# Performance work log

Hardware: AMD Instinct MI355X
Metric: run time of the kernel (lower is better)

The kernel has to match this reference:

```python
import jax, jax.numpy as jnp
import numpy as np

B, T, D = 4, 2048, 1024
H = 16
HD = D // H


def setup_inputs() -> dict:
    key = jax.random.key(0)
    ks = jax.random.split(key, 6)
    s = 1.0 / np.sqrt(D)
    return {
        "inputs": jax.random.normal(ks[0], (B, T, D), dtype=jnp.float32),
        "Wq": jax.random.normal(ks[1], (D, D), dtype=jnp.float32) * s,
        "Wk": jax.random.normal(ks[2], (D, D), dtype=jnp.float32) * s,
        "Wv": jax.random.normal(ks[3], (D, D), dtype=jnp.float32) * s,
        "Wo": jax.random.normal(ks[4], (D, D), dtype=jnp.float32) * s,
        "bo": jax.random.normal(ks[5], (D,), dtype=jnp.float32) * 0.01,
    }


def reference(inputs, Wq, Wk, Wv, Wo, bo):
    # qkv projections (torch Linear: x @ W.T; here W stored as [in, out])
    q = jnp.einsum('btd,de->bte', inputs, Wq).reshape(B, T, H, HD)
    k = jnp.einsum('btd,de->bte', inputs, Wk).reshape(B, T, H, HD)
    v = jnp.einsum('btd,de->bte', inputs, Wv).reshape(B, T, H, HD)
    # scores [B,H,T,T]
    scores = jnp.einsum('bqhd,bkhd->bhqk', q, k)
    causal = jnp.triu(jnp.ones((T, T), dtype=bool), k=1)
    scores = jnp.where(causal, -jnp.inf, scores)
    attn = jax.nn.softmax(scores / jnp.sqrt(jnp.float32(HD)), axis=-1)
    ctx = jnp.einsum('bhqk,bkhd->bqhd', attn, v).reshape(B, T, D)
    return jnp.einsum('btd,de->bte', ctx, Wo) + bo
```

## Files before the change

kernel.cpp:

```cpp
#include <hip/hip_runtime.h>

typedef unsigned short u16;
typedef __attribute__((ext_vector_type(8))) __bf16 bf16x8;
typedef __attribute__((ext_vector_type(4))) float f32x4;
typedef __attribute__((ext_vector_type(16))) float f32x16;

#define B_  4
#define T_  2048
#define D_  1024
#define H_  16
#define HD_ 64
#define M_  (B_*T_)

__device__ __forceinline__ u16 f2bf(float x) {
  unsigned u = __float_as_uint(x);
  return (u16)((u + 0x7FFFu + ((u >> 16) & 1u)) >> 16);
}

__device__ __forceinline__ unsigned cvtpk(float lo, float hi) {
  unsigned r;
  asm("v_cvt_pk_bf16_f32 %0, %1, %2" : "=v"(r) : "v"(lo), "v"(hi));
  return r;
}

__device__ __forceinline__ void async16(const void* g, void* lds) {
  __builtin_amdgcn_global_load_lds((__attribute__((address_space(1))) void*)g,
                                   (__attribute__((address_space(3))) void*)lds,
                                   16, 0, 0);
}

__global__ void k_convert_x(const float* __restrict__ x, u16* __restrict__ xb) {
  const int n4 = M_ * D_ / 4;
  for (int i = blockIdx.x * blockDim.x + threadIdx.x; i < n4; i += gridDim.x * blockDim.x) {
    float4 v = ((const float4*)x)[i];
    u16 o0 = f2bf(v.x), o1 = f2bf(v.y), o2 = f2bf(v.z), o3 = f2bf(v.w);
    unsigned lo = (unsigned)o0 | ((unsigned)o1 << 16);
    unsigned hi = (unsigned)o2 | ((unsigned)o3 << 16);
    ((uint2*)xb)[i] = make_uint2(lo, hi);
  }
}

__global__ void k_transpose_w(const float* __restrict__ Wq, const float* __restrict__ Wk,
                              const float* __restrict__ Wv, const float* __restrict__ Wo,
                              u16* __restrict__ WqkvT, u16* __restrict__ WoT) {
  __shared__ float tile[32][33];
  const float* W; u16* Wt;
  switch (blockIdx.z) {
    case 0:  W = Wq; Wt = WqkvT;               break;
    case 1:  W = Wk; Wt = WqkvT + 1024 * D_;   break;
    case 2:  W = Wv; Wt = WqkvT + 2048 * D_;   break;
    default: W = Wo; Wt = WoT;                 break;
  }
  int tx = threadIdx.x & 31, ty = threadIdx.x >> 5;
  int k0 = blockIdx.y * 32, n0 = blockIdx.x * 32;
#pragma unroll
  for (int i = 0; i < 4; i++) {
    int r = ty + i * 8;
    tile[r][tx] = W[(k0 + r) * D_ + n0 + tx];
  }
  __syncthreads();
#pragma unroll
  for (int i = 0; i < 4; i++) {
    int r = ty + i * 8;
    Wt[(n0 + r) * D_ + k0 + tx] = f2bf(tile[tx][r]);
  }
}

__device__ __forceinline__ void gemm_tile(const u16* __restrict__ A, const u16* __restrict__ Bt,
                                          u16* Alds, u16* Blds,
                                          int m0, int n0, f32x4 acc[4][4]) {
  const int tid = threadIdx.x;
  const int l = tid & 63, w = tid >> 6;
  const int wm = (w >> 1) * 64, wn = (w & 1) * 64;
  const int lr = l & 15, lg = l >> 4;
  const f32x4 fz = {0.f, 0.f, 0.f, 0.f};
#pragma unroll
  for (int i = 0; i < 4; i++)
#pragma unroll
    for (int j = 0; j < 4; j++) acc[i][j] = fz;

  for (int kt = 0; kt < 1024; kt += 64) {
    __syncthreads();
#pragma unroll
    for (int i = 0; i < 4; i++) {
      int ch = tid + 256 * i;
      int r = ch >> 3, c8 = ch & 7;
      async16(A  + (m0 + r) * 1024 + kt + c8 * 8, Alds + ch * 8);
      async16(Bt + (n0 + r) * 1024 + kt + c8 * 8, Blds + ch * 8);
    }
    __syncthreads();
#pragma unroll
    for (int kk = 0; kk < 64; kk += 32) {
      bf16x8 af[4], bfr[4];
#pragma unroll
      for (int mi = 0; mi < 4; mi++)
        af[mi] = *(const bf16x8*)(Alds + (wm + mi * 16 + lr) * 64 + kk + lg * 8);
#pragma unroll
      for (int ni = 0; ni < 4; ni++)
        bfr[ni] = *(const bf16x8*)(Blds + (wn + ni * 16 + lr) * 64 + kk + lg * 8);
#pragma unroll
      for (int mi = 0; mi < 4; mi++)
#pragma unroll
        for (int ni = 0; ni < 4; ni++)
          acc[mi][ni] = __builtin_amdgcn_mfma_f32_16x16x32_bf16(af[mi], bfr[ni], acc[mi][ni], 0, 0, 0);
    }
  }
}

__global__ __launch_bounds__(256) void k_gemm_qkv(const u16* __restrict__ X,
                                                  const u16* __restrict__ WqkvT,
                                                  u16* __restrict__ Q, u16* __restrict__ K, u16* __restrict__ V) {
  __shared__ u16 Alds[128 * 64];
  __shared__ u16 Blds[128 * 64];
  int m0 = blockIdx.y * 128, n0 = blockIdx.x * 128;
  int reg = n0 >> 10;
  u16* Out = (reg == 0) ? Q : (reg == 1) ? K : V;
  int nb = n0 & 1023;
  f32x4 acc[4][4];
  gemm_tile(X, WqkvT, Alds, Blds, m0, n0, acc);
  const int l = threadIdx.x & 63, w = threadIdx.x >> 6;
  const int wm = (w >> 1) * 64, wn = (w & 1) * 64;
  const int lr = l & 15, lg = l >> 4;
#pragma unroll
  for (int mi = 0; mi < 4; mi++)
#pragma unroll
    for (int ni = 0; ni < 4; ni++)
#pragma unroll
      for (int r = 0; r < 4; r++) {
        int row = m0 + wm + mi * 16 + lg * 4 + r;
        int col = nb + wn + ni * 16 + lr;
        Out[row * D_ + col] = f2bf(acc[mi][ni][r]);
      }
}

__global__ __launch_bounds__(256) void k_gemm_out(const u16* __restrict__ Cx, const u16* __restrict__ WoT,
                                                  const float* __restrict__ bo, float* __restrict__ out) {
  __shared__ u16 Alds[128 * 64];
  __shared__ u16 Blds[128 * 64];
  int m0 = blockIdx.y * 128, n0 = blockIdx.x * 128;
  f32x4 acc[4][4];
  gemm_tile(Cx, WoT, Alds, Blds, m0, n0, acc);
  const int l = threadIdx.x & 63, w = threadIdx.x >> 6;
  const int wm = (w >> 1) * 64, wn = (w & 1) * 64;
  const int lr = l & 15, lg = l >> 4;
#pragma unroll
  for (int mi = 0; mi < 4; mi++)
#pragma unroll
    for (int ni = 0; ni < 4; ni++)
#pragma unroll
      for (int r = 0; r < 4; r++) {
        int row = m0 + wm + mi * 16 + lg * 4 + r;
        int col = n0 + wn + ni * 16 + lr;
        out[row * D_ + col] = acc[mi][ni][r] + bo[col];
      }
}

__global__ void k_transpose_v(const u16* __restrict__ V, u16* __restrict__ Vt) {
  __shared__ u16 tile[64][65];
  int bh = blockIdx.y;
  int b = bh >> 4, h = bh & 15;
  int t0 = blockIdx.x * 64;
  int tx = threadIdx.x & 63, ty = threadIdx.x >> 6;
#pragma unroll
  for (int i = 0; i < 16; i++) {
    int r = ty + i * 4;
    tile[r][tx] = V[(b * T_ + t0 + r) * D_ + h * HD_ + tx];
  }
  __syncthreads();
#pragma unroll
  for (int i = 0; i < 16; i++) {
    int d = ty + i * 4;
    Vt[((size_t)(bh * HD_ + d)) * T_ + t0 + tx] = tile[tx][d];
  }
}

__global__ __launch_bounds__(256) void k_flash(const u16* __restrict__ Q, const u16* __restrict__ Kb,
                                               const u16* __restrict__ Vt, u16* __restrict__ ctx) {
  __shared__ u16 Klds[64 * 64];
  __shared__ u16 Vlds[64 * 64];
  int lin = blockIdx.x + blockIdx.y * gridDim.x;
  int swz = (lin & 7) * 128 + (lin >> 3);
  const int qb = swz & 15, bh = swz >> 4;
  const int b = bh >> 4, h = bh & 15;
  const int qs = qb * 128;
  const int tid = threadIdx.x, l = tid & 63, w = tid >> 6;
  const int q5 = l & 31, hi = l >> 5;
  const int wrow = qs + w * 32;
  const int qa = wrow + q5;
  const float EA = 0.18033688f, EB = -17.312340f;

  const u16* Qrow = Q + (size_t)(b * T_ + qa) * D_ + h * HD_;
  bf16x8 aQ[4];
#pragma unroll
  for (int kc = 0; kc < 4; kc++)
    aQ[kc] = *(const bf16x8*)(Qrow + kc * 16 + hi * 8);

  f32x16 o[2] = {};
  float psum = 0.f;

  for (int kv0 = 0; kv0 <= qs + 64; kv0 += 64) {
    __syncthreads();
#pragma unroll
    for (int i = 0; i < 2; i++) {
      int ch = tid + 256 * i;
      int r = ch >> 3, c8 = (ch & 7) ^ (r & 7);
      async16(Kb + (size_t)(b * T_ + kv0 + r) * D_ + h * HD_ + c8 * 8, Klds + ch * 8);
      async16(Vt + (size_t)(bh * HD_ + r) * T_ + kv0 + c8 * 8, Vlds + ch * 8);
    }
    __syncthreads();

    if (kv0 > wrow + 31) continue;
    const bool anymask = (kv0 + 63 > wrow);

#pragma unroll
    for (int kt = 0; kt < 2; kt++) {
      f32x16 st = {};
#pragma unroll
      for (int kc = 0; kc < 4; kc++) {
        const int row = kt * 32 + q5;
        bf16x8 kf = *(const bf16x8*)(Klds + row * 64 + (((kc * 2 + hi) ^ (row & 7))) * 8);
        st = __builtin_amdgcn_mfma_f32_32x32x16_bf16(kf, aQ[kc], st, 0, 0, 0);
      }
      float e[16];
#pragma unroll
      for (int r = 0; r < 16; r++) {
        int kva = kv0 + kt * 32 + (r & 3) + 8 * (r >> 2) + 4 * hi;
        float ev = exp2f(fmaf(st[r], EA, EB));
        if (anymask && kva > qa) ev = 0.f;
        e[r] = ev;
        psum += ev;
      }
#pragma unroll
      for (int eh = 0; eh < 2; eh++) {
        unsigned a0 = cvtpk(e[eh * 8 + 0], e[eh * 8 + 1]);
        unsigned a1 = cvtpk(e[eh * 8 + 2], e[eh * 8 + 3]);
        unsigned b0 = cvtpk(e[eh * 8 + 4], e[eh * 8 + 5]);
        unsigned b1 = cvtpk(e[eh * 8 + 6], e[eh * 8 + 7]);
        asm volatile("v_permlane32_swap_b32 %0, %1" : "+v"(a0), "+v"(b0));
        asm volatile("v_permlane32_swap_b32 %0, %1" : "+v"(a1), "+v"(b1));
        union { unsigned u[4]; bf16x8 v; } pf;
        pf.u[0] = a0; pf.u[1] = a1; pf.u[2] = b0; pf.u[3] = b1;
        const int ch = kt * 4 + eh * 2 + hi;
#pragma unroll
        for (int dt = 0; dt < 2; dt++) {
          const int vrow = dt * 32 + q5;
          bf16x8 vf = *(const bf16x8*)(Vlds + vrow * 64 + ((ch ^ (vrow & 7))) * 8);
          o[dt] = __builtin_amdgcn_mfma_f32_32x32x16_bf16(vf, pf.v, o[dt], 0, 0, 0);
        }
      }
    }
  }

  psum += __shfl_xor(psum, 32, 64);
  const float inv = 1.f / psum;
  u16* crow = ctx + (size_t)(b * T_ + qa) * D_ + h * HD_;
#pragma unroll
  for (int dt = 0; dt < 2; dt++)
#pragma unroll
    for (int r = 0; r < 16; r += 2) {
      int d = dt * 32 + (r & 3) + 8 * (r >> 2) + 4 * hi;
      unsigned pk2 = cvtpk(o[dt][r] * inv, o[dt][r + 1] * inv);
      *(unsigned*)(crow + d) = pk2;
    }
}

extern "C" void kernel_launch(void* const* d_in, const int* in_sizes, int n_in,
                              void* d_out, int out_size, void* d_ws, size_t ws_size,
                              hipStream_t stream) {
  const float* x  = (const float*)d_in[0];
  const float* Wq = (const float*)d_in[1];
  const float* Wk = (const float*)d_in[2];
  const float* Wv = (const float*)d_in[3];
  const float* Wo = (const float*)d_in[4];
  const float* bo = (const float*)d_in[5];
  float* out = (float*)d_out;

  char* ws = (char*)d_ws;
  u16* Xb     = (u16*)(ws);
  u16* WqkvT  = (u16*)(ws + 16777216);
  u16* WoT    = (u16*)(ws + 23068672);
  u16* Qb     = (u16*)(ws + 25165824);
  u16* Kb     = (u16*)(ws + 41943040);
  u16* Vb     = (u16*)(ws + 58720256);
  u16* Vtb    = (u16*)(ws + 75497472);
  u16* Cb     = (u16*)(ws + 92274688);

  k_convert_x<<<dim3(2048), dim3(256), 0, stream>>>(x, Xb);
  k_transpose_w<<<dim3(32, 32, 4), dim3(256), 0, stream>>>(Wq, Wk, Wv, Wo, WqkvT, WoT);
  k_gemm_qkv<<<dim3(24, 64), dim3(256), 0, stream>>>(Xb, WqkvT, Qb, Kb, Vb);
  k_transpose_v<<<dim3(32, 64), dim3(256), 0, stream>>>(Vb, Vtb);
  k_flash<<<dim3(16, 64), dim3(256), 0, stream>>>(Qb, Kb, Vtb, Cb);
  k_gemm_out<<<dim3(8, 64), dim3(256), 0, stream>>>(Cb, WoT, bo, out);
}
```

Baseline: 312.0 us.

## Double-buffer K/V tiles and pair causal query blocks per workgroup in flash kernel

The flash attention kernel now double-buffers K and V tiles in LDS, issuing async loads for the next tile before computing the current one and using explicit vmcnt waits. Each workgroup processes two query blocks (qb and 15-qb), which balances the causal triangle's work and halves the grid to 512 blocks. It also raises wave priority around the MFMA section and widens the output stores. The cost is twice the LDS footprint and lower occupancy, plus fewer workgroups to spread across CUs.

```diff
diff --git a/kernel.cpp b/kernel.cpp
--- a/kernel.cpp
+++ b/kernel.cpp
@@ -4,6 +4,7 @@
 typedef __attribute__((ext_vector_type(8))) __bf16 bf16x8;
 typedef __attribute__((ext_vector_type(4))) float f32x4;
 typedef __attribute__((ext_vector_type(16))) float f32x16;
+typedef __attribute__((ext_vector_type(4))) unsigned u32x4;
 
 #define B_  4
 #define T_  2048
@@ -176,92 +177,126 @@
 
 __global__ __launch_bounds__(256) void k_flash(const u16* __restrict__ Q, const u16* __restrict__ Kb,
                                                const u16* __restrict__ Vt, u16* __restrict__ ctx) {
-  __shared__ u16 Klds[64 * 64];
-  __shared__ u16 Vlds[64 * 64];
-  int lin = blockIdx.x + blockIdx.y * gridDim.x;
-  int swz = (lin & 7) * 128 + (lin >> 3);
-  const int qb = swz & 15, bh = swz >> 4;
+  __shared__ u16 Klds0[64 * 64], Klds1[64 * 64];
+  __shared__ u16 Vlds0[64 * 64], Vlds1[64 * 64];
+  const int lin = blockIdx.x;
+  const int swz = (lin & 7) * 64 + (lin >> 3);
+  const int bh = swz >> 3, pr = swz & 7;
   const int b = bh >> 4, h = bh & 15;
-  const int qs = qb * 128;
   const int tid = threadIdx.x, l = tid & 63, w = tid >> 6;
   const int q5 = l & 31, hi = l >> 5;
-  const int wrow = qs + w * 32;
-  const int qa = wrow + q5;
   const float EA = 0.18033688f, EB = -17.312340f;
 
-  const u16* Qrow = Q + (size_t)(b * T_ + qa) * D_ + h * HD_;
-  bf16x8 aQ[4];
-#pragma unroll
-  for (int kc = 0; kc < 4; kc++)
-    aQ[kc] = *(const bf16x8*)(Qrow + kc * 16 + hi * 8);
-
-  f32x16 o[2] = {};
-  float psum = 0.f;
-
-  for (int kv0 = 0; kv0 <= qs + 64; kv0 += 64) {
-    __syncthreads();
-#pragma unroll
-    for (int i = 0; i < 2; i++) {
-      int ch = tid + 256 * i;
-      int r = ch >> 3, c8 = (ch & 7) ^ (r & 7);
-      async16(Kb + (size_t)(b * T_ + kv0 + r) * D_ + h * HD_ + c8 * 8, Klds + ch * 8);
-      async16(Vt + (size_t)(bh * HD_ + r) * T_ + kv0 + c8 * 8, Vlds + ch * 8);
+  const int ch0 = tid, ch1 = tid + 256;
+  const int r0 = ch0 >> 3, c80 = (ch0 & 7) ^ (r0 & 7);
+  const int r1 = ch1 >> 3, c81 = (ch1 & 7) ^ (r1 & 7);
+  const u16* kb0 = Kb + (size_t)(b * T_ + r0) * D_ + h * HD_ + c80 * 8;
+  const u16* kb1 = Kb + (size_t)(b * T_ + r1) * D_ + h * HD_ + c81 * 8;
+  const u16* vb0 = Vt + (size_t)(bh * HD_ + r0) * T_ + c80 * 8;
+  const u16* vb1 = Vt + (size_t)(bh * HD_ + r1) * T_ + c81 * 8;
+
+  for (int ph = 0; ph < 2; ph++) {
+    const int qb = ph ? (15 - pr) : pr;
+    const int qs = qb * 128;
+    const int nt = 2 * qb + 2;
+    const int wrow = qs + w * 32;
+    const int qa = wrow + q5;
+
+    const u16* Qrow = Q + (size_t)(b * T_ + qa) * D_ + h * HD_;
+    bf16x8 aQ[4];
+#pragma unroll
+    for (int kc = 0; kc < 4; kc++)
+      aQ[kc] = *(const bf16x8*)(Qrow + kc * 16 + hi * 8);
+
+    f32x16 o[2] = {};
+    float psum = 0.f;
+
+    __builtin_amdgcn_s_barrier();
+    async16(kb0, Klds0 + ch0 * 8);
+    async16(kb1, Klds0 + ch1 * 8);
+    async16(vb0, Vlds0 + ch0 * 8);
+    async16(vb1, Vlds0 + ch1 * 8);
+
+    for (int t = 0; t < nt; t++) {
+      const int cur = t & 1;
+      if (t + 1 < nt) {
+        const size_t ko = (size_t)(t + 1) * 64 * D_;
+        const size_t vo = (size_t)(t + 1) * 64;
+        u16* kl = cur ? Klds0 : Klds1;
+        u16* vl = cur ? Vlds0 : Vlds1;
+        async16(kb0 + ko, kl + ch0 * 8);
+        async16(kb1 + ko, kl + ch1 * 8);
+        async16(vb0 + vo, vl + ch0 * 8);
+        async16(vb1 + vo, vl + ch1 * 8);
+        asm volatile("s_waitcnt vmcnt(4)" ::: "memory");
+      } else {
+        asm volatile("s_waitcnt vmcnt(0)" ::: "memory");
+      }
+      __builtin_amdgcn_s_barrier();
+      __builtin_amdgcn_sched_barrier(0);
+
+      const int kv0 = t * 64;
+      if (kv0 <= wrow + 31) {
+        __builtin_amdgcn_s_setprio(1);
+        const bool anymask = (kv0 + 63 > wrow);
+        const u16* Kl = cur ? Klds1 : Klds0;
+        const u16* Vl = cur ? Vlds1 : Vlds0;
+#pragma unroll
+        for (int kt = 0; kt < 2; kt++) {
+          f32x16 st = {};
+          const int row = kt * 32 + q5;
+#pragma unroll
+          for (int kc = 0; kc < 4; kc++) {
+            bf16x8 kf = *(const bf16x8*)(Kl + row * 64 + (((kc * 2 + hi) ^ (row & 7))) * 8);
+            st = __builtin_amdgcn_mfma_f32_32x32x16_bf16(kf, aQ[kc], st, 0, 0, 0);
+          }
+          float e[16];
+#pragma unroll
+          for (int r = 0; r < 16; r++) {
+            int kva = kv0 + kt * 32 + (r & 3) + 8 * (r >> 2) + 4 * hi;
+            float ev = exp2f(fmaf(st[r], EA, EB));
+            if (anymask && kva > qa) ev = 0.f;
+            e[r] = ev;
+            psum += ev;
+          }
+#pragma unroll
+          for (int eh = 0; eh < 2; eh++) {
+            unsigned a0 = cvtpk(e[eh * 8 + 0], e[eh * 8 + 1]);
+            unsigned a1 = cvtpk(e[eh * 8 + 2], e[eh * 8 + 3]);
+            unsigned b0 = cvtpk(e[eh * 8 + 4], e[eh * 8 + 5]);
+            unsigned b1 = cvtpk(e[eh * 8 + 6], e[eh * 8 + 7]);
+            asm volatile("v_permlane32_swap_b32 %0, %1" : "+v"(a0), "+v"(b0));
+            asm volatile("v_permlane32_swap_b32 %0, %1" : "+v"(a1), "+v"(b1));
+            u32x4 pu; pu.x = a0; pu.y = a1; pu.z = b0; pu.w = b1;
+            bf16x8 pf = __builtin_bit_cast(bf16x8, pu);
+            const int ch = kt * 4 + eh * 2 + hi;
+#pragma unroll
+            for (int dt = 0; dt < 2; dt++) {
+              const int vrow = dt * 32 + q5;
+              bf16x8 vf = *(const bf16x8*)(Vl + vrow * 64 + ((ch ^ (vrow & 7))) * 8);
+              o[dt] = __builtin_amdgcn_mfma_f32_32x32x16_bf16(vf, pf, o[dt], 0, 0, 0);
+            }
+          }
+        }
+        __builtin_amdgcn_s_setprio(0);
+      }
+      __builtin_amdgcn_s_barrier();
     }
-    __syncthreads();
-
-    if (kv0 > wrow + 31) continue;
-    const bool anymask = (kv0 + 63 > wrow);
-
-#pragma unroll
-    for (int kt = 0; kt < 2; kt++) {
-      f32x16 st = {};
-#pragma unroll
-      for (int kc = 0; kc < 4; kc++) {
-        const int row = kt * 32 + q5;
-        bf16x8 kf = *(const bf16x8*)(Klds + row * 64 + (((kc * 2 + hi) ^ (row & 7))) * 8);
-        st = __builtin_amdgcn_mfma_f32_32x32x16_bf16(kf, aQ[kc], st, 0, 0, 0);
-      }
-      float e[16];
-#pragma unroll
-      for (int r = 0; r < 16; r++) {
-        int kva = kv0 + kt * 32 + (r & 3) + 8 * (r >> 2) + 4 * hi;
-        float ev = exp2f(fmaf(st[r], EA, EB));
-        if (anymask && kva > qa) ev = 0.f;
-        e[r] = ev;
-        psum += ev;
-      }
-#pragma unroll
-      for (int eh = 0; eh < 2; eh++) {
-        unsigned a0 = cvtpk(e[eh * 8 + 0], e[eh * 8 + 1]);
-        unsigned a1 = cvtpk(e[eh * 8 + 2], e[eh * 8 + 3]);
-        unsigned b0 = cvtpk(e[eh * 8 + 4], e[eh * 8 + 5]);
-        unsigned b1 = cvtpk(e[eh * 8 + 6], e[eh * 8 + 7]);
-        asm volatile("v_permlane32_swap_b32 %0, %1" : "+v"(a0), "+v"(b0));
-        asm volatile("v_permlane32_swap_b32 %0, %1" : "+v"(a1), "+v"(b1));
-        union { unsigned u[4]; bf16x8 v; } pf;
-        pf.u[0] = a0; pf.u[1] = a1; pf.u[2] = b0; pf.u[3] = b1;
-        const int ch = kt * 4 + eh * 2 + hi;
-#pragma unroll
-        for (int dt = 0; dt < 2; dt++) {
-          const int vrow = dt * 32 + q5;
-          bf16x8 vf = *(const bf16x8*)(Vlds + vrow * 64 + ((ch ^ (vrow & 7))) * 8);
-          o[dt] = __builtin_amdgcn_mfma_f32_32x32x16_bf16(vf, pf.v, o[dt], 0, 0, 0);
-        }
-      }
-    }
-  }
-
-  psum += __shfl_xor(psum, 32, 64);
-  const float inv = 1.f / psum;
-  u16* crow = ctx + (size_t)(b * T_ + qa) * D_ + h * HD_;
-#pragma unroll
-  for (int dt = 0; dt < 2; dt++)
-#pragma unroll
-    for (int r = 0; r < 16; r += 2) {
-      int d = dt * 32 + (r & 3) + 8 * (r >> 2) + 4 * hi;
-      unsigned pk2 = cvtpk(o[dt][r] * inv, o[dt][r + 1] * inv);
-      *(unsigned*)(crow + d) = pk2;
-    }
+
+    psum += __shfl_xor(psum, 32, 64);
+    const float inv = 1.f / psum;
+    u16* crow = ctx + (size_t)(b * T_ + qa) * D_ + h * HD_;
+#pragma unroll
+    for (int dt = 0; dt < 2; dt++)
+#pragma unroll
+      for (int rr = 0; rr < 16; rr += 4) {
+        int d = dt * 32 + (rr >> 2) * 8 + 4 * hi;
+        uint2 s;
+        s.x = cvtpk(o[dt][rr + 0] * inv, o[dt][rr + 1] * inv);
+        s.y = cvtpk(o[dt][rr + 2] * inv, o[dt][rr + 3] * inv);
+        *(uint2*)(crow + d) = s;
+      }
+  }
 }
 
 extern "C" void kernel_launch(void* const* d_in, const int* in_sizes, int n_in,
@@ -289,6 +324,6 @@
   k_transpose_w<<<dim3(32, 32, 4), dim3(256), 0, stream>>>(Wq, Wk, Wv, Wo, WqkvT, WoT);
   k_gemm_qkv<<<dim3(24, 64), dim3(256), 0, stream>>>(Xb, WqkvT, Qb, Kb, Vb);
   k_transpose_v<<<dim3(32, 64), dim3(256), 0, stream>>>(Vb, Vtb);
-  k_flash<<<dim3(16, 64), dim3(256), 0, stream>>>(Qb, Kb, Vtb, Cb);
+  k_flash<<<dim3(512), dim3(256), 0, stream>>>(Qb, Kb, Vtb, Cb);
   k_gemm_out<<<dim3(8, 64), dim3(256), 0, stream>>>(Cb, WoT, bo, out);
 }
```

New measurement: 298.3 us. -4.4%, faster.

## Restructure flash attention: split KV across two waves, pair causal blocks, drop LDS staging

Applied to the files above, without the earlier changes.

The flash kernel now runs 128-thread blocks where each block processes two 32-row query tiles (p and 63-p) to balance causal work. The two waves split KV subtiles odd/even and combine partial outputs through LDS. K and V fragments are read straight from global memory instead of being staged into LDS with async copies, and exp2f is replaced by raw v_exp_f32. This is meant to remove barrier overhead and causal load imbalance, at the cost of uncoalesced, cache-reliant global reads and an extra LDS reduction.

```diff
diff --git a/kernel.cpp b/kernel.cpp
--- a/kernel.cpp
+++ b/kernel.cpp
@@ -4,6 +4,7 @@
 typedef __attribute__((ext_vector_type(8))) __bf16 bf16x8;
 typedef __attribute__((ext_vector_type(4))) float f32x4;
 typedef __attribute__((ext_vector_type(16))) float f32x16;
+typedef __attribute__((ext_vector_type(4))) unsigned u32x4;
 
 #define B_  4
 #define T_  2048
@@ -20,6 +21,12 @@
 __device__ __forceinline__ unsigned cvtpk(float lo, float hi) {
   unsigned r;
   asm("v_cvt_pk_bf16_f32 %0, %1, %2" : "=v"(r) : "v"(lo), "v"(hi));
+  return r;
+}
+
+__device__ __forceinline__ float expraw(float x) {
+  float r;
+  asm("v_exp_f32 %0, %1" : "=v"(r) : "v"(x));
   return r;
 }
 
@@ -174,61 +181,58 @@
   }
 }
 
-__global__ __launch_bounds__(256) void k_flash(const u16* __restrict__ Q, const u16* __restrict__ Kb,
-                                               const u16* __restrict__ Vt, u16* __restrict__ ctx) {
-  __shared__ u16 Klds[64 * 64];
-  __shared__ u16 Vlds[64 * 64];
-  int lin = blockIdx.x + blockIdx.y * gridDim.x;
-  int swz = (lin & 7) * 128 + (lin >> 3);
-  const int qb = swz & 15, bh = swz >> 4;
+__global__ __launch_bounds__(128, 4) void k_flash(const u16* __restrict__ Q, const u16* __restrict__ Kb,
+                                                  const u16* __restrict__ Vt, u16* __restrict__ ctx) {
+  __shared__ float xo[2][2][64][17];
+  __shared__ float xps[2][2][64];
+  const int lin = blockIdx.x;
+  const int c = lin & 7, idx = lin >> 3;
+  const int bh = c * 8 + (idx >> 5);
+  const int p = idx & 31;
   const int b = bh >> 4, h = bh & 15;
-  const int qs = qb * 128;
   const int tid = threadIdx.x, l = tid & 63, w = tid >> 6;
   const int q5 = l & 31, hi = l >> 5;
-  const int wrow = qs + w * 32;
-  const int qa = wrow + q5;
   const float EA = 0.18033688f, EB = -17.312340f;
 
-  const u16* Qrow = Q + (size_t)(b * T_ + qa) * D_ + h * HD_;
-  bf16x8 aQ[4];
-#pragma unroll
-  for (int kc = 0; kc < 4; kc++)
-    aQ[kc] = *(const bf16x8*)(Qrow + kc * 16 + hi * 8);
-
-  f32x16 o[2] = {};
-  float psum = 0.f;
-
-  for (int kv0 = 0; kv0 <= qs + 64; kv0 += 64) {
-    __syncthreads();
-#pragma unroll
-    for (int i = 0; i < 2; i++) {
-      int ch = tid + 256 * i;
-      int r = ch >> 3, c8 = (ch & 7) ^ (r & 7);
-      async16(Kb + (size_t)(b * T_ + kv0 + r) * D_ + h * HD_ + c8 * 8, Klds + ch * 8);
-      async16(Vt + (size_t)(bh * HD_ + r) * T_ + kv0 + c8 * 8, Vlds + ch * 8);
-    }
-    __syncthreads();
-
-    if (kv0 > wrow + 31) continue;
-    const bool anymask = (kv0 + 63 > wrow);
-
-#pragma unroll
-    for (int kt = 0; kt < 2; kt++) {
+  const u16* Kbase  = Kb + (size_t)(b * T_ + q5) * D_ + h * HD_ + hi * 8;
+  const u16* Vbase0 = Vt + (size_t)(bh * HD_ + q5) * T_ + hi * 8;
+  const u16* Vbase1 = Vbase0 + (size_t)32 * T_;
+
+  for (int ph = 0; ph < 2; ph++) {
+    const int qb = ph ? (63 - p) : p;
+    const int qs = qb * 32;
+    const int qa = qs + q5;
+
+    const u16* Qrow = Q + (size_t)(b * T_ + qa) * D_ + h * HD_;
+    bf16x8 aQ[4];
+#pragma unroll
+    for (int kc = 0; kc < 4; kc++)
+      aQ[kc] = *(const bf16x8*)(Qrow + kc * 16 + hi * 8);
+
+    f32x16 o0 = {}, o1 = {};
+    float ps0 = 0.f, ps1 = 0.f, ps2 = 0.f, ps3 = 0.f;
+
+    auto subtile = [&](int s, bool mask) __attribute__((always_inline)) {
       f32x16 st = {};
+      const u16* kp = Kbase + (size_t)s * 32 * D_;
 #pragma unroll
       for (int kc = 0; kc < 4; kc++) {
-        const int row = kt * 32 + q5;
-        bf16x8 kf = *(const bf16x8*)(Klds + row * 64 + (((kc * 2 + hi) ^ (row & 7))) * 8);
+        bf16x8 kf = *(const bf16x8*)(kp + kc * 16);
         st = __builtin_amdgcn_mfma_f32_32x32x16_bf16(kf, aQ[kc], st, 0, 0, 0);
       }
       float e[16];
 #pragma unroll
       for (int r = 0; r < 16; r++) {
-        int kva = kv0 + kt * 32 + (r & 3) + 8 * (r >> 2) + 4 * hi;
-        float ev = exp2f(fmaf(st[r], EA, EB));
-        if (anymask && kva > qa) ev = 0.f;
+        float ev = expraw(fmaf(st[r], EA, EB));
+        if (mask) {
+          int kva = s * 32 + (r & 3) + 8 * (r >> 2) + 4 * hi;
+          if (kva > qa) ev = 0.f;
+        }
         e[r] = ev;
-        psum += ev;
+      }
+#pragma unroll
+      for (int r = 0; r < 16; r += 4) {
+        ps0 += e[r]; ps1 += e[r + 1]; ps2 += e[r + 2]; ps3 += e[r + 3];
       }
 #pragma unroll
       for (int eh = 0; eh < 2; eh++) {
@@ -238,30 +242,42 @@
         unsigned b1 = cvtpk(e[eh * 8 + 6], e[eh * 8 + 7]);
         asm volatile("v_permlane32_swap_b32 %0, %1" : "+v"(a0), "+v"(b0));
         asm volatile("v_permlane32_swap_b32 %0, %1" : "+v"(a1), "+v"(b1));
-        union { unsigned u[4]; bf16x8 v; } pf;
-        pf.u[0] = a0; pf.u[1] = a1; pf.u[2] = b0; pf.u[3] = b1;
-        const int ch = kt * 4 + eh * 2 + hi;
-#pragma unroll
-        for (int dt = 0; dt < 2; dt++) {
-          const int vrow = dt * 32 + q5;
-          bf16x8 vf = *(const bf16x8*)(Vlds + vrow * 64 + ((ch ^ (vrow & 7))) * 8);
-          o[dt] = __builtin_amdgcn_mfma_f32_32x32x16_bf16(vf, pf.v, o[dt], 0, 0, 0);
-        }
-      }
+        u32x4 pu; pu.x = a0; pu.y = a1; pu.z = b0; pu.w = b1;
+        bf16x8 pf = __builtin_bit_cast(bf16x8, pu);
+        const size_t vo = (size_t)s * 32 + eh * 16;
+        bf16x8 vf0 = *(const bf16x8*)(Vbase0 + vo);
+        bf16x8 vf1 = *(const bf16x8*)(Vbase1 + vo);
+        o0 = __builtin_amdgcn_mfma_f32_32x32x16_bf16(vf0, pf, o0, 0, 0, 0);
+        o1 = __builtin_amdgcn_mfma_f32_32x32x16_bf16(vf1, pf, o1, 0, 0, 0);
+      }
+    };
+
+    for (int s = w; s < qb; s += 2) subtile(s, false);
+    if ((qb & 1) == w) subtile(qb, true);
+
+    float ps = (ps0 + ps1) + (ps2 + ps3);
+    const f32x16 give = w ? o0 : o1;
+#pragma unroll
+    for (int i = 0; i < 16; i++) xo[ph][w][l][i] = give[i];
+    xps[ph][w][l] = ps;
+    __syncthreads();
+    f32x16 keep = w ? o1 : o0;
+#pragma unroll
+    for (int i = 0; i < 16; i++) keep[i] += xo[ph][1 - w][l][i];
+    float pst = ps + xps[ph][1 - w][l];
+    pst += __shfl_xor(pst, 32, 64);
+    const float inv = 1.f / pst;
+
+    u16* crow = ctx + (size_t)(b * T_ + qa) * D_ + h * HD_ + w * 32;
+#pragma unroll
+    for (int g = 0; g < 4; g++) {
+      int d = g * 8 + 4 * hi;
+      uint2 so;
+      so.x = cvtpk(keep[g * 4 + 0] * inv, keep[g * 4 + 1] * inv);
+      so.y = cvtpk(keep[g * 4 + 2] * inv, keep[g * 4 + 3] * inv);
+      *(uint2*)(crow + d) = so;
     }
   }
-
-  psum += __shfl_xor(psum, 32, 64);
-  const float inv = 1.f / psum;
-  u16* crow = ctx + (size_t)(b * T_ + qa) * D_ + h * HD_;
-#pragma unroll
-  for (int dt = 0; dt < 2; dt++)
-#pragma unroll
-    for (int r = 0; r < 16; r += 2) {
-      int d = dt * 32 + (r & 3) + 8 * (r >> 2) + 4 * hi;
-      unsigned pk2 = cvtpk(o[dt][r] * inv, o[dt][r + 1] * inv);
-      *(unsigned*)(crow + d) = pk2;
-    }
 }
 
 extern "C" void kernel_launch(void* const* d_in, const int* in_sizes, int n_in,
@@ -289,6 +305,6 @@
   k_transpose_w<<<dim3(32, 32, 4), dim3(256), 0, stream>>>(Wq, Wk, Wv, Wo, WqkvT, WoT);
   k_gemm_qkv<<<dim3(24, 64), dim3(256), 0, stream>>>(Xb, WqkvT, Qb, Kb, Vb);
   k_transpose_v<<<dim3(32, 64), dim3(256), 0, stream>>>(Vb, Vtb);
-  k_flash<<<dim3(16, 64), dim3(256), 0, stream>>>(Qb, Kb, Vtb, Cb);
+  k_flash<<<dim3(2048), dim3(128), 0, stream>>>(Qb, Kb, Vtb, Cb);
   k_gemm_out<<<dim3(8, 64), dim3(256), 0, stream>>>(Cb, WoT, bo, out);
 }
```

Measured after the change: 338.5 us. 8.5% more time.
